# Performance work log

Measured on AMD Instinct MI355X. Metric: run time of the kernel, lower is better.

## Reference

```python
import jax, jax.numpy as jnp
import numpy as np

BATCH_SIZE = 512
N_PARTS = 4
TEMP_FAC = 0.1
D = 4096
EPS = 1e-6


def _static_indices():
    # bs and factor per the n_parts==4, batch_size!=12 branch
    bs = 4 * BATCH_SIZE
    factor = 10 * N_PARTS
    pos = np.arange(bs)
    active = pos[pos % (3 * N_PARTS) < N_PARTS]            # positions that contribute
    # i1..i6 = (pos + k*n_parts) % bs for k = 0..5
    I = (active[:, None] + np.arange(6)[None, :] * N_PARTS) % bs   # (P, 6)
    # denominator indices removed: (pos + k*n_parts) % bs for k = 0..factor*n_parts-1
    offs = (active[:, None] + np.arange(factor * N_PARTS)[None, :] * N_PARTS) % bs
    M = np.ones((active.shape[0], bs), dtype=np.float32)
    M[np.arange(active.shape[0])[:, None], offs] = 0.0     # (P, bs) denominator mask
    return I, M

_I, _M = _static_indices()
# symmetrical-loss pairs: (i1,i2),(i2,i3),(i1,i4),(i4,i5),(i5,i6),(i2,i5),(i3,i6)
_PAIRS = [(0, 1), (1, 2), (0, 3), (3, 4), (4, 5), (1, 4), (2, 5)]


def setup_inputs() -> dict:
    key = jax.random.key(0)
    reg_pred = jax.random.normal(key, (4 * BATCH_SIZE, D), dtype=jnp.float32)
    return {"reg_pred": reg_pred}


def reference(reg_pred):
    I = jnp.asarray(_I)
    M = jnp.asarray(_M)
    norms = jnp.linalg.norm(reg_pred, axis=1)              # (bs,)
    # torch CosineSimilarity: dot / max(||a||*||b||, eps)
    gram = reg_pred @ reg_pred.T                           # (bs, bs)
    S = gram / jnp.maximum(norms[:, None] * norms[None, :], EPS) / TEMP_FAC
    E = jnp.exp(S)                                         # (bs, bs)
    # denominator exp-sums for each anchor role k at each active position p
    Dsum = jnp.einsum('pkb,pb->pk', E[I], M)               # (P, 6)
    total = jnp.float32(0.0)
    for a, b in _PAIRS:
        num = S[I[:, a], I[:, b]]                          # (P,)
        en = jnp.exp(num)
        total = total + jnp.sum(-jnp.log(en / (en + Dsum[:, a]))
                                - jnp.log(en / (en + Dsum[:, b])))
    return total / (6 * BATCH_SIZE)
```

## Files before the change

kernel.cpp:

```cpp
#include <hip/hip_runtime.h>
#include <hip/hip_bf16.h>
#include <stdint.h>

#define NROWS 2048
#define DIM   4096
#define NACT  684
#define INV_TEMP 10.0f
#define NTILE 136
#define KSPLIT 8
#define KSEG  512
#define FP8_SCALE 16.0f
#define PART_SCALE (1.0f / 256.0f)

#define WAITCNT_VM0   0x0F70
#define WAITCNT_VM2   0x0F72
#define WAITCNT_VM4   0x0F74

typedef __attribute__((ext_vector_type(4))) float floatx4;
typedef __attribute__((ext_vector_type(8))) short shortx8;
typedef __attribute__((ext_vector_type(8))) unsigned short ushortx8;

static __device__ __forceinline__ unsigned short f32_to_bf16(float f) {
  union { float f; unsigned int u; } v; v.f = f;
  unsigned int u = v.u;
  unsigned int r = u + 0x7fffu + ((u >> 16) & 1u);
  return (unsigned short)(r >> 16);
}
static __device__ __forceinline__ float bf16_to_f32(unsigned short u) {
  union { unsigned int u; float f; } v; v.u = ((unsigned int)u) << 16;
  return v.f;
}

__global__ __launch_bounds__(256) void k_normconv_fp8(const float* __restrict__ X,
                                                      unsigned char* __restrict__ Yq) {
  const int row = blockIdx.x;
  const float4* xr = (const float4*)(X + (size_t)row * DIM);
  float4 v[4];
  float s = 0.f;
#pragma unroll
  for (int t = 0; t < 4; t++) {
    float4 w = xr[threadIdx.x * 4 + t];
    v[t] = w;
    s += w.x * w.x + w.y * w.y + w.z * w.z + w.w * w.w;
  }
#pragma unroll
  for (int off = 32; off > 0; off >>= 1) s += __shfl_down(s, off, 64);
  __shared__ float wsum[4];
  if ((threadIdx.x & 63) == 0) wsum[threadIdx.x >> 6] = s;
  __syncthreads();
  const float total = wsum[0] + wsum[1] + wsum[2] + wsum[3];
  const float sc = FP8_SCALE / fmaxf(sqrtf(total), 1e-30f);
  uint4 o;
  unsigned int r0;
  r0 = __builtin_amdgcn_cvt_pk_fp8_f32(v[0].x * sc, v[0].y * sc, 0, false);
  o.x = __builtin_amdgcn_cvt_pk_fp8_f32(v[0].z * sc, v[0].w * sc, r0, true);
  r0 = __builtin_amdgcn_cvt_pk_fp8_f32(v[1].x * sc, v[1].y * sc, 0, false);
  o.y = __builtin_amdgcn_cvt_pk_fp8_f32(v[1].z * sc, v[1].w * sc, r0, true);
  r0 = __builtin_amdgcn_cvt_pk_fp8_f32(v[2].x * sc, v[2].y * sc, 0, false);
  o.z = __builtin_amdgcn_cvt_pk_fp8_f32(v[2].z * sc, v[2].w * sc, r0, true);
  r0 = __builtin_amdgcn_cvt_pk_fp8_f32(v[3].x * sc, v[3].y * sc, 0, false);
  o.w = __builtin_amdgcn_cvt_pk_fp8_f32(v[3].z * sc, v[3].w * sc, r0, true);
  ((uint4*)(Yq + (size_t)row * DIM))[threadIdx.x] = o;
}

__global__ __launch_bounds__(256) void k_gemm_sym(const unsigned char* __restrict__ Yq,
                                                  unsigned short* __restrict__ P) {
  __shared__ __attribute__((aligned(16))) unsigned char lds[3 * 8192];
  const int t = blockIdx.x;
  const int kz = blockIdx.y;
  int ti = 0, rem = t;
  while (rem >= 16 - ti) { rem -= 16 - ti; ti++; }
  const int tj = ti + rem;
  const int row0 = ti * 128;
  const int col0 = tj * 128;
  const int kbase = kz * KSEG;

  const int tid  = threadIdx.x;
  const int lane = tid & 63;
  const int wave = tid >> 6;
  const int wr = wave >> 1;
  const int wc = wave & 1;

  floatx4 zero = {0.f, 0.f, 0.f, 0.f};
  floatx4 acc[4][4];
#pragma unroll
  for (int i = 0; i < 4; i++)
#pragma unroll
    for (int j = 0; j < 4; j++) acc[i][j] = zero;

  const unsigned char* gA = Yq + (size_t)(row0 + (tid >> 1)) * DIM + kbase + (tid & 1) * 16;
  const unsigned char* gB = Yq + (size_t)(col0 + (tid >> 1)) * DIM + kbase + (tid & 1) * 16;

  const int fr  = lane & 15;
  const int fc8 = (lane >> 4) * 8;

#define ISSUE(st, koff)                                                                \
  do {                                                                                 \
    __builtin_amdgcn_global_load_lds(                                                  \
        (const __attribute__((address_space(1))) void*)(gA + (koff)),                  \
        (__attribute__((address_space(3))) void*)(lds + (st) * 8192 + tid * 16),       \
        16, 0, 0);                                                                     \
    __builtin_amdgcn_global_load_lds(                                                  \
        (const __attribute__((address_space(1))) void*)(gB + (koff)),                  \
        (__attribute__((address_space(3))) void*)(lds + (st) * 8192 + 4096 + tid * 16),\
        16, 0, 0);                                                                     \
  } while (0)

#define COMPUTE(st)                                                                    \
  do {                                                                                 \
    const unsigned char* bA = lds + (st) * 8192;                                       \
    const unsigned char* bB = bA + 4096;                                               \
    long long af[4], bf[4];                                                            \
    _Pragma("unroll")                                                                  \
    for (int mi = 0; mi < 4; mi++)                                                     \
      af[mi] = *(const long long*)(bA + (wr * 64 + mi * 16 + fr) * 32 + fc8);          \
    _Pragma("unroll")                                                                  \
    for (int ni = 0; ni < 4; ni++)                                                     \
      bf[ni] = *(const long long*)(bB + (wc * 64 + ni * 16 + fr) * 32 + fc8);          \
    _Pragma("unroll")                                                                  \
    for (int mi = 0; mi < 4; mi++)                                                     \
      _Pragma("unroll")                                                                \
      for (int ni = 0; ni < 4; ni++)                                                   \
        acc[mi][ni] = __builtin_amdgcn_mfma_f32_16x16x32_fp8_fp8(af[mi], bf[ni],       \
                                                                 acc[mi][ni], 0, 0, 0);\
  } while (0)

  ISSUE(0, 0);
  ISSUE(1, 32);
#pragma unroll
  for (int k = 0; k < 16; k++) {
    const int cur = k % 3;
    if (k < 14) {
      ISSUE((k + 2) % 3, (k + 2) * 32);
      __builtin_amdgcn_s_waitcnt(WAITCNT_VM4);
    } else if (k == 14) {
      __builtin_amdgcn_s_waitcnt(WAITCNT_VM2);
    } else {
      __builtin_amdgcn_s_waitcnt(WAITCNT_VM0);
    }
    __builtin_amdgcn_sched_barrier(0);
    __builtin_amdgcn_s_barrier();
    COMPUTE(cur);
    if (k < 15) {
      __builtin_amdgcn_s_barrier();
      __builtin_amdgcn_sched_barrier(0);
    }
  }

#undef ISSUE
#undef COMPUTE

  unsigned short* dst = P + (size_t)(t * KSPLIT + kz) * 16384;
  const int cc  = lane & 15;
  const int cr4 = (lane >> 4) * 4;
#pragma unroll
  for (int mi = 0; mi < 4; mi++) {
    const int row = wr * 64 + mi * 16 + cr4;
#pragma unroll
    for (int ni = 0; ni < 4; ni++) {
      const int col = wc * 64 + ni * 16 + cc;
      unsigned int d0 = (unsigned int)f32_to_bf16(acc[mi][ni][0] * PART_SCALE) |
                        ((unsigned int)f32_to_bf16(acc[mi][ni][1] * PART_SCALE) << 16);
      unsigned int d1 = (unsigned int)f32_to_bf16(acc[mi][ni][2] * PART_SCALE) |
                        ((unsigned int)f32_to_bf16(acc[mi][ni][3] * PART_SCALE) << 16);
      uint2 v; v.x = d0; v.y = d1;
      *(uint2*)(dst + (size_t)col * 128 + row) = v;
    }
  }
}

__global__ __launch_bounds__(256) void k_combine(const unsigned short* __restrict__ P,
                                                 float* __restrict__ S,
                                                 float* __restrict__ T) {
  __shared__ float tileS[32][132];
  __shared__ float tileE[32][132];
  const int t = blockIdx.x;
  const int h = blockIdx.y;
  int ti = 0, rem = t;
  while (rem >= 16 - ti) { rem -= 16 - ti; ti++; }
  const int tj = ti + rem;
  const int gr = ti * 128, gc = tj * 128;
  const int c0 = h * 32;
  const int tid = threadIdx.x;
  const int cl = tid >> 3;
  const int q  = tid & 7;

  float acc[16];
#pragma unroll
  for (int j = 0; j < 16; j++) acc[j] = 0.f;
#pragma unroll
  for (int kz = 0; kz < KSPLIT; kz++) {
    const ushortx8* p = (const ushortx8*)(P + (size_t)(t * KSPLIT + kz) * 16384 +
                                          (size_t)(c0 + cl) * 128 + q * 16);
#pragma unroll
    for (int c = 0; c < 2; c++) {
      ushortx8 u = p[c];
#pragma unroll
      for (int e = 0; e < 8; e++) acc[c * 8 + e] += bf16_to_f32((unsigned short)u[e]);
    }
  }
  float cs = 0.f;
#pragma unroll
  for (int j = 0; j < 16; j++) {
    float v = acc[j] * INV_TEMP;
    acc[j] = v;
    float ev = __expf(v);
    tileS[cl][q * 16 + j] = v;
    tileE[cl][q * 16 + j] = ev;
    cs += ev;
  }
  {
    floatx4* srow = (floatx4*)(S + (size_t)(gc + c0 + cl) * NROWS + gr + q * 16);
#pragma unroll
    for (int u = 0; u < 4; u++) {
      floatx4 w = {acc[u * 4], acc[u * 4 + 1], acc[u * 4 + 2], acc[u * 4 + 3]};
      srow[u] = w;
    }
  }
  cs += __shfl_xor(cs, 1, 64);
  cs += __shfl_xor(cs, 2, 64);
  cs += __shfl_xor(cs, 4, 64);
  if (q == 0) atomicAdd(&T[gc + c0 + cl], cs);

  if (ti != tj) {
    __syncthreads();
    const int r = tid >> 1;
    const int hh = tid & 1;
    float rs = 0.f;
    float vals[16];
#pragma unroll
    for (int e = 0; e < 16; e++) {
      vals[e] = tileS[hh * 16 + e][r];
      rs += tileE[hh * 16 + e][r];
    }
    floatx4* drow = (floatx4*)(S + (size_t)(gr + r) * NROWS + gc + c0 + hh * 16);
#pragma unroll
    for (int u = 0; u < 4; u++) {
      floatx4 w = {vals[u * 4], vals[u * 4 + 1], vals[u * 4 + 2], vals[u * 4 + 3]};
      drow[u] = w;
    }
    rs += __shfl_xor(rs, 1, 64);
    if (hh == 0) atomicAdd(&T[gr + r], rs);
  }
}

__global__ __launch_bounds__(256) void k_normconv(const float* __restrict__ X,
                                                  unsigned short* __restrict__ Y) {
  const int row = blockIdx.x;
  const float4* xr = (const float4*)(X + (size_t)row * DIM);
  float4 v[4];
  float s = 0.f;
#pragma unroll
  for (int t = 0; t < 4; t++) {
    float4 w = xr[threadIdx.x + t * 256];
    v[t] = w;
    s += w.x * w.x + w.y * w.y + w.z * w.z + w.w * w.w;
  }
#pragma unroll
  for (int off = 32; off > 0; off >>= 1) s += __shfl_down(s, off, 64);
  __shared__ float wsum[4];
  if ((threadIdx.x & 63) == 0) wsum[threadIdx.x >> 6] = s;
  __syncthreads();
  const float total = wsum[0] + wsum[1] + wsum[2] + wsum[3];
  const float inv = 1.0f / fmaxf(sqrtf(total), 1e-30f);
  ushort4* yr = (ushort4*)(Y + (size_t)row * DIM);
#pragma unroll
  for (int t = 0; t < 4; t++) {
    float4 w = v[t];
    ushort4 o;
    o.x = f32_to_bf16(w.x * inv);
    o.y = f32_to_bf16(w.y * inv);
    o.z = f32_to_bf16(w.z * inv);
    o.w = f32_to_bf16(w.w * inv);
    yr[threadIdx.x + t * 256] = o;
  }
}

__global__ __launch_bounds__(256) void k_gemm(const unsigned short* __restrict__ Y,
                                              float* __restrict__ S) {
  __shared__ __attribute__((aligned(16))) unsigned short sA[128 * 32];
  __shared__ __attribute__((aligned(16))) unsigned short sB[128 * 32];
  const int tid  = threadIdx.x;
  const int lane = tid & 63;
  const int wave = tid >> 6;
  const int wr = wave >> 1;
  const int wc = wave & 1;
  const int row0 = blockIdx.y * 128;
  const int col0 = blockIdx.x * 128;

  floatx4 zero = {0.f, 0.f, 0.f, 0.f};
  floatx4 acc[4][4];
#pragma unroll
  for (int i = 0; i < 4; i++)
#pragma unroll
    for (int j = 0; j < 4; j++) acc[i][j] = zero;

  const int sr = tid >> 2;
  const int sc = (tid & 3) * 8;
  const unsigned short* gA0 = Y + (size_t)(row0 + sr) * DIM + sc;
  const unsigned short* gA1 = gA0 + (size_t)64 * DIM;
  const unsigned short* gB0 = Y + (size_t)(col0 + sr) * DIM + sc;
  const unsigned short* gB1 = gB0 + (size_t)64 * DIM;

  const int fr = lane & 15;
  const int fc = (lane >> 4) * 8;

  for (int k0 = 0; k0 < DIM; k0 += 32) {
    __builtin_amdgcn_global_load_lds(
        (const __attribute__((address_space(1))) void*)(gA0 + k0),
        (__attribute__((address_space(3))) void*)(sA + tid * 8), 16, 0, 0);
    __builtin_amdgcn_global_load_lds(
        (const __attribute__((address_space(1))) void*)(gA1 + k0),
        (__attribute__((address_space(3))) void*)(sA + 2048 + tid * 8), 16, 0, 0);
    __builtin_amdgcn_global_load_lds(
        (const __attribute__((address_space(1))) void*)(gB0 + k0),
        (__attribute__((address_space(3))) void*)(sB + tid * 8), 16, 0, 0);
    __builtin_amdgcn_global_load_lds(
        (const __attribute__((address_space(1))) void*)(gB1 + k0),
        (__attribute__((address_space(3))) void*)(sB + 2048 + tid * 8), 16, 0, 0);
    __syncthreads();

    shortx8 af[4], bf[4];
#pragma unroll
    for (int mi = 0; mi < 4; mi++)
      af[mi] = *(const shortx8*)(sA + (wr * 64 + mi * 16 + fr) * 32 + fc);
#pragma unroll
    for (int ni = 0; ni < 4; ni++)
      bf[ni] = *(const shortx8*)(sB + (wc * 64 + ni * 16 + fr) * 32 + fc);
#pragma unroll
    for (int mi = 0; mi < 4; mi++)
#pragma unroll
      for (int ni = 0; ni < 4; ni++)
        acc[mi][ni] = __builtin_amdgcn_mfma_f32_16x16x32_bf16(af[mi], bf[ni], acc[mi][ni], 0, 0, 0);
    __syncthreads();
  }

  const int cc  = lane & 15;
  const int cr4 = (lane >> 4) * 4;
#pragma unroll
  for (int mi = 0; mi < 4; mi++) {
    const int row = row0 + wr * 64 + mi * 16 + cr4;
#pragma unroll
    for (int ni = 0; ni < 4; ni++) {
      const int col = col0 + wc * 64 + ni * 16 + cc;
      float* dst = S + (size_t)row * NROWS + col;
#pragma unroll
      for (int r = 0; r < 4; r++) dst[(size_t)r * NROWS] = acc[mi][ni][r] * INV_TEMP;
    }
  }
}

__global__ __launch_bounds__(256) void k_rowsum(const float* __restrict__ S,
                                                float* __restrict__ T) {
  const int row = blockIdx.x;
  const float* sr = S + (size_t)row * NROWS;
  float s = 0.f;
  for (int b = threadIdx.x; b < NROWS; b += 256) s += __expf(sr[b]);
#pragma unroll
  for (int off = 32; off > 0; off >>= 1) s += __shfl_down(s, off, 64);
  __shared__ float wsum[4];
  if ((threadIdx.x & 63) == 0) wsum[threadIdx.x >> 6] = s;
  __syncthreads();
  if (threadIdx.x == 0) T[row] = wsum[0] + wsum[1] + wsum[2] + wsum[3];
}

__global__ __launch_bounds__(64) void k_dsum(const float* __restrict__ S,
                                             const float* __restrict__ T,
                                             float* __restrict__ Ds) {
  const int p = blockIdx.x;
  const int k = blockIdx.y;
  const int a = 12 * (p >> 2) + (p & 3);
  const int lane = threadIdx.x;
  const int row = (a + 4 * k) & (NROWS - 1);
  const float* sr = S + (size_t)row * NROWS;
  float s = 0.f;
  for (int j = lane; j < 160; j += 64) s += __expf(sr[(a + 4 * j) & (NROWS - 1)]);
#pragma unroll
  for (int off = 32; off > 0; off >>= 1) s += __shfl_down(s, off, 64);
  if (lane == 0) Ds[p * 6 + k] = T[row] - s;
}

__global__ __launch_bounds__(256) void k_final(const float* __restrict__ S,
                                               const float* __restrict__ Ds,
                                               float* __restrict__ out) {
  const int pa[7] = {0, 1, 0, 3, 4, 1, 2};
  const int pb[7] = {1, 2, 3, 4, 5, 4, 5};
  const int idx = blockIdx.x * 256 + threadIdx.x;
  float s = 0.f;
  if (idx < NACT * 7) {
    const int p = idx / 7;
    const int q = idx - p * 7;
    const int a0 = 12 * (p >> 2) + (p & 3);
    const int ra = (a0 + 4 * pa[q]) & (NROWS - 1);
    const int rb = (a0 + 4 * pb[q]) & (NROWS - 1);
    const float num = S[(size_t)ra * NROWS + rb];
    const float en = __expf(num);
    s = __logf(en + Ds[p * 6 + pa[q]]) + __logf(en + Ds[p * 6 + pb[q]]) - 2.f * num;
  }
#pragma unroll
  for (int off = 32; off > 0; off >>= 1) s += __shfl_down(s, off, 64);
  if ((threadIdx.x & 63) == 0) atomicAdd(out, s * (1.0f / (6.0f * 512.0f)));
}

extern "C" void kernel_launch(void* const* d_in, const int* in_sizes, int n_in,
                              void* d_out, int out_size, void* d_ws, size_t ws_size,
                              hipStream_t stream) {
  const float* X = (const float*)d_in[0];
  char* ws = (char*)d_ws;
  float* S = (float*)(ws + (size_t)16 * 1024 * 1024);
  float* out = (float*)d_out;

  const size_t pOff = (size_t)32 * 1024 * 1024;
  const size_t pBytes = (size_t)NTILE * KSPLIT * 16384 * 2;
  const size_t needA = pOff + pBytes + 8192 + NACT * 6 * 4 + 256;

  hipMemsetAsync(out, 0, sizeof(float), stream);

  if (ws_size >= needA) {
    unsigned char* Yq = (unsigned char*)ws;
    unsigned short* P = (unsigned short*)(ws + pOff);
    float* T  = (float*)(ws + pOff + pBytes);
    float* Ds = (float*)(ws + pOff + pBytes + 8192);
    hipMemsetAsync(T, 0, NROWS * sizeof(float), stream);
    hipLaunchKernelGGL(k_normconv_fp8, dim3(NROWS), dim3(256), 0, stream, X, Yq);
    hipLaunchKernelGGL(k_gemm_sym, dim3(NTILE, KSPLIT), dim3(256), 0, stream, Yq, P);
    hipLaunchKernelGGL(k_combine, dim3(NTILE, 4), dim3(256), 0, stream, P, S, T);
    hipLaunchKernelGGL(k_dsum, dim3(NACT, 6), dim3(64), 0, stream, S, T, Ds);
    hipLaunchKernelGGL(k_final, dim3((NACT * 7 + 255) / 256), dim3(256), 0, stream, S, Ds, out);
  } else {
    unsigned short* Y = (unsigned short*)ws;
    float* T  = (float*)(ws + pOff);
    float* Ds = (float*)(ws + pOff + 8192);
    hipLaunchKernelGGL(k_normconv, dim3(NROWS), dim3(256), 0, stream, X, Y);
    hipLaunchKernelGGL(k_gemm, dim3(16, 16), dim3(256), 0, stream, Y, S);
    hipLaunchKernelGGL(k_rowsum, dim3(NROWS), dim3(256), 0, stream, S, T);
    hipLaunchKernelGGL(k_dsum, dim3(NACT, 6), dim3(64), 0, stream, S, T, Ds);
    hipLaunchKernelGGL(k_final, dim3((NACT * 7 + 255) / 256), dim3(256), 0, stream, S, Ds, out);
  }
}
```

Before: 127.4 us.

## Deepen GEMM LDS pipeline to four stages, remap grid, vectorize dsum gathers

The symmetric FP8 GEMM now uses a four-buffer LDS ring with three loads in flight instead of two, with waitcnt thresholds adjusted to match. It also flattens the grid so the eight K-split blocks of a tile are adjacent in launch order, which should improve L2 reuse of the same A/B rows. The dsum kernel replaces strided scalar gathers with float4 loads and a lane select. The costs are more LDS per block, which may lower occupancy, and dsum now reads four times the bytes it needs per element.

```diff
diff --git a/kernel.cpp b/kernel.cpp
--- a/kernel.cpp
+++ b/kernel.cpp
@@ -15,6 +15,7 @@
 #define WAITCNT_VM0   0x0F70
 #define WAITCNT_VM2   0x0F72
 #define WAITCNT_VM4   0x0F74
+#define WAITCNT_VM6   0x0F76
 
 typedef __attribute__((ext_vector_type(4))) float floatx4;
 typedef __attribute__((ext_vector_type(8))) short shortx8;
@@ -65,9 +66,10 @@
 
 __global__ __launch_bounds__(256) void k_gemm_sym(const unsigned char* __restrict__ Yq,
                                                   unsigned short* __restrict__ P) {
-  __shared__ __attribute__((aligned(16))) unsigned char lds[3 * 8192];
-  const int t = blockIdx.x;
-  const int kz = blockIdx.y;
+  __shared__ __attribute__((aligned(16))) unsigned char lds[4 * 8192];
+  const int bid = blockIdx.x;
+  const int kz = bid & 7;
+  const int t  = bid >> 3;
   int ti = 0, rem = t;
   while (rem >= 16 - ti) { rem -= 16 - ti; ti++; }
   const int tj = ti + rem;
@@ -127,11 +129,14 @@
 
   ISSUE(0, 0);
   ISSUE(1, 32);
+  ISSUE(2, 64);
 #pragma unroll
   for (int k = 0; k < 16; k++) {
-    const int cur = k % 3;
-    if (k < 14) {
-      ISSUE((k + 2) % 3, (k + 2) * 32);
+    const int cur = k & 3;
+    if (k < 13) {
+      ISSUE((k + 3) & 3, (k + 3) * 32);
+      __builtin_amdgcn_s_waitcnt(WAITCNT_VM6);
+    } else if (k == 13) {
       __builtin_amdgcn_s_waitcnt(WAITCNT_VM4);
     } else if (k == 14) {
       __builtin_amdgcn_s_waitcnt(WAITCNT_VM2);
@@ -372,9 +377,22 @@
   const int a = 12 * (p >> 2) + (p & 3);
   const int lane = threadIdx.x;
   const int row = (a + 4 * k) & (NROWS - 1);
-  const float* sr = S + (size_t)row * NROWS;
+  const int m = a >> 2;
+  const int c = a & 3;
+  const float4* sr4 = (const float4*)(S + (size_t)row * NROWS);
   float s = 0.f;
-  for (int j = lane; j < 160; j += 64) s += __expf(sr[(a + 4 * j) & (NROWS - 1)]);
+  {
+    float4 v0 = sr4[(m + lane) & 511];
+    float4 v1 = sr4[(m + 64 + lane) & 511];
+    float e0 = c == 0 ? v0.x : c == 1 ? v0.y : c == 2 ? v0.z : v0.w;
+    float e1 = c == 0 ? v1.x : c == 1 ? v1.y : c == 2 ? v1.z : v1.w;
+    s += __expf(e0) + __expf(e1);
+    if (lane < 32) {
+      float4 v2 = sr4[(m + 128 + lane) & 511];
+      float e2 = c == 0 ? v2.x : c == 1 ? v2.y : c == 2 ? v2.z : v2.w;
+      s += __expf(e2);
+    }
+  }
 #pragma unroll
   for (int off = 32; off > 0; off >>= 1) s += __shfl_down(s, off, 64);
   if (lane == 0) Ds[p * 6 + k] = T[row] - s;
@@ -423,7 +441,7 @@
     float* Ds = (float*)(ws + pOff + pBytes + 8192);
     hipMemsetAsync(T, 0, NROWS * sizeof(float), stream);
     hipLaunchKernelGGL(k_normconv_fp8, dim3(NROWS), dim3(256), 0, stream, X, Yq);
-    hipLaunchKernelGGL(k_gemm_sym, dim3(NTILE, KSPLIT), dim3(256), 0, stream, Yq, P);
+    hipLaunchKernelGGL(k_gemm_sym, dim3(NTILE * KSPLIT), dim3(256), 0, stream, Yq, P);
     hipLaunchKernelGGL(k_combine, dim3(NTILE, 4), dim3(256), 0, stream, P, S, T);
     hipLaunchKernelGGL(k_dsum, dim3(NACT, 6), dim3(64), 0, stream, S, T, Ds);
     hipLaunchKernelGGL(k_final, dim3((NACT * 7 + 255) / 256), dim3(256), 0, stream, S, Ds, out);
```

New measurement: 127.7 us. About the same (+0.2%).
